# Kernel optimization log

Measured on AMD Instinct MI355X. Metric: run time of the kernel, lower is better.

## Reference

```python
import jax, jax.numpy as jnp
import numpy as np

N = 100000      # nodes
E = 3200000     # edges (avg degree 32)
IN = 256        # in_channels
HID = 32        # hidden (hard-coded in module)
OUT = 40        # out_channels / classes
BN_EPS = 1e-5


def gcn_conv(x, W, b, src, dst, n):
    # PyG GCNConv: h = x @ W; add self-loops; symmetric norm D^-1/2 A D^-1/2; aggregate; + bias
    h = x @ W                                   # [n, d_out]
    loop = jnp.arange(n)
    s = jnp.concatenate([src, loop])            # [E+n]
    d = jnp.concatenate([dst, loop])
    deg = jax.ops.segment_sum(jnp.ones_like(d, dtype=h.dtype), d, num_segments=n)
    dinv = jnp.where(deg > 0, jax.lax.rsqrt(deg), 0.0)
    norm = dinv[s] * dinv[d]                    # [E+n]
    msg = h[s] * norm[:, None]                  # gather + scale
    return jax.ops.segment_sum(msg, d, num_segments=n) + b


def setup_inputs() -> dict:
    key = jax.random.key(0)
    k = jax.random.split(key, 4)
    x = jax.random.normal(k[0], (N, IN), dtype=jnp.float32)
    edge_index = jax.random.randint(k[1], (2, E), 0, N, dtype=jnp.int64)
    W1 = jax.random.normal(k[2], (IN, HID), dtype=jnp.float32) / np.float32(np.sqrt(IN))
    b1 = jnp.zeros((HID,), jnp.float32)
    W2 = jax.random.normal(k[3], (HID, OUT), dtype=jnp.float32) / np.float32(np.sqrt(HID))
    b2 = jnp.zeros((OUT,), jnp.float32)
    return {"x": x, "edge_index": edge_index, "W1": W1, "b1": b1, "W2": W2, "b2": b2}


def reference(x, edge_index, W1, b1, W2, b2):
    src, dst = edge_index[0], edge_index[1]
    h = jax.nn.elu(gcn_conv(x, W1, b1, src, dst, N))
    # BatchNorm1d created fresh each forward: batch stats, gamma=1, beta=0 (biased var)
    mean = jnp.mean(h, axis=0)
    var = jnp.mean((h - mean) ** 2, axis=0)
    h = (h - mean) * jax.lax.rsqrt(var + BN_EPS)
    h = jax.nn.relu(h)
    # Dropout(p=0.2): identity in eval / deterministic reference
    out = gcn_conv(h, W2, b2, src, dst, N)
    return jax.nn.log_softmax(out, axis=-1)
```

## Files before the change

kernel.cpp:

```cpp
#include <hip/hip_runtime.h>
#include <math.h>

typedef unsigned int uint;
typedef unsigned short ushort;
typedef float v2f __attribute__((ext_vector_type(2)));

__device__ __forceinline__ v2f fp8lo_to_f32(uint u) {
    return __builtin_amdgcn_cvt_pk_f32_fp8((int)u, false);
}
__device__ __forceinline__ ushort f32x2_to_fp8(float a, float b) {
    return (ushort)(__builtin_amdgcn_cvt_pk_fp8_f32(a, b, 0, false) & 0xffff);
}

#define NBU 49
#define CELL 9216
#define BUCK_CAP (8 * CELL)

__global__ __launch_bounds__(256) void k_bin(
    const int* __restrict__ src, const int* __restrict__ dst,
    int* __restrict__ cur, uint* __restrict__ ebuf, int E) {
    __shared__ int hist[NBU], base_[NBU], off[NBU];
    int tid = threadIdx.x;
    if (tid < NBU) { hist[tid] = 0; off[tid] = 0; }
    __syncthreads();
    int e0 = blockIdx.x * 4096 + tid;
    int s_[16], d_[16];
#pragma unroll
    for (int j = 0; j < 16; ++j) {
        int e = e0 + j * 256;
        if (e < E) {
            s_[j] = src[e]; d_[j] = dst[e];
            atomicAdd(&hist[d_[j] >> 11], 1);
        } else d_[j] = -1;
    }
    __syncthreads();
    int seg = blockIdx.x & 7;
    if (tid < NBU && hist[tid])
        base_[tid] = atomicAdd(&cur[tid * 8 + seg], hist[tid]);
    __syncthreads();
#pragma unroll
    for (int j = 0; j < 16; ++j) {
        if (d_[j] >= 0) {
            int b = d_[j] >> 11;
            int p = base_[b] + atomicAdd(&off[b], 1);
            if (p < CELL)
                ebuf[(size_t)(b * 8 + seg) * CELL + p] =
                    ((uint)(d_[j] & 2047) << 17) | (uint)s_[j];
        }
    }
}

__global__ __launch_bounds__(1024) void k_sort(
    const int* __restrict__ cur, const uint* __restrict__ ebuf,
    uint* __restrict__ csr, int* __restrict__ rowstart, int* __restrict__ deg,
    float* __restrict__ dinv, int n) {
    __shared__ int cnt[2048];
    __shared__ int part[1024];
    int tid = threadIdx.x, b = blockIdx.x;
    cnt[2 * tid] = 0; cnt[2 * tid + 1] = 0;
    __syncthreads();
    int lens[8];
    for (int s = 0; s < 8; ++s) {
        int len = cur[b * 8 + s]; if (len > CELL) len = CELL; lens[s] = len;
        const uint* ep = ebuf + (size_t)(b * 8 + s) * CELL;
        for (int i = tid; i < len; i += 1024)
            atomicAdd(&cnt[ep[i] >> 17], 1);
    }
    __syncthreads();
    int c0 = cnt[2 * tid], c1 = cnt[2 * tid + 1];
    part[tid] = c0 + c1;
    __syncthreads();
    for (int o = 1; o < 1024; o <<= 1) {
        int v = (tid >= o) ? part[tid - o] : 0;
        __syncthreads();
        part[tid] += v;
        __syncthreads();
    }
    int excl = (tid == 0) ? 0 : part[tid - 1];
    int bucketBase = b * BUCK_CAP;
    int node0 = b * 2048 + 2 * tid;
    if (node0 < n) {
        rowstart[node0] = bucketBase + excl;
        deg[node0] = c0;
        dinv[node0] = rsqrtf((float)c0 + 1.0f);
    }
    if (node0 + 1 < n) {
        rowstart[node0 + 1] = bucketBase + excl + c0;
        deg[node0 + 1] = c1;
        dinv[node0 + 1] = rsqrtf((float)c1 + 1.0f);
    }
    __syncthreads();
    cnt[2 * tid] = excl;
    cnt[2 * tid + 1] = excl + c0;
    __syncthreads();
    for (int s = 0; s < 8; ++s) {
        const uint* ep = ebuf + (size_t)(b * 8 + s) * CELL;
        int len = lens[s];
        for (int i = tid; i < len; i += 1024) {
            uint v = ep[i];
            int p = atomicAdd(&cnt[v >> 17], 1);
            csr[bucketBase + p] = v & 0x1FFFFu;
        }
    }
}


__global__ __launch_bounds__(256) void k_gemm1(
    const float* __restrict__ x, const float* __restrict__ W,
    const float* __restrict__ dinv, ushort* __restrict__ h8, int n) {
    __shared__ float part[4 * 32 * 64];
    int lane = threadIdx.x & 63;
    int wv = __builtin_amdgcn_readfirstlane(threadIdx.x >> 6);
    int node0 = blockIdx.x * 64;
    int node = node0 + lane;
    int koff = wv * 64;

    float acc[32];
#pragma unroll
    for (int c = 0; c < 32; ++c) acc[c] = 0.f;
    if (node < n) {
        const float4* xr = (const float4*)(x + (size_t)node * 256 + koff);
#pragma unroll 4
        for (int j4 = 0; j4 < 16; ++j4) {
            float4 xv = xr[j4];
            const float* w0 = W + (koff + j4 * 4) * 32;
#pragma unroll
            for (int c = 0; c < 32; ++c) acc[c] += xv.x * w0[c];
#pragma unroll
            for (int c = 0; c < 32; ++c) acc[c] += xv.y * w0[32 + c];
#pragma unroll
            for (int c = 0; c < 32; ++c) acc[c] += xv.z * w0[64 + c];
#pragma unroll
            for (int c = 0; c < 32; ++c) acc[c] += xv.w * w0[96 + c];
        }
    }
    float* pw = part + wv * 2048 + lane;
#pragma unroll
    for (int c = 0; c < 32; ++c) pw[c * 64] = acc[c];
    __syncthreads();

    int rn = threadIdx.x >> 2;
    int cq = threadIdx.x & 3;
    int dnode = node0 + rn;
    if (dnode < n) {
        float di = dinv[dnode];
        ushort us[4];
#pragma unroll
        for (int half = 0; half < 4; ++half) {
            float v0 = 0.f, v1 = 0.f;
#pragma unroll
            for (int w = 0; w < 4; ++w) {
                v0 += part[w * 2048 + (cq * 8 + half * 2 + 0) * 64 + rn];
                v1 += part[w * 2048 + (cq * 8 + half * 2 + 1) * 64 + rn];
            }
            us[half] = f32x2_to_fp8(v0 * di, v1 * di);
        }
        uint2 p;
        p.x = (uint)us[0] | ((uint)us[1] << 16);
        p.y = (uint)us[2] | ((uint)us[3] << 16);
        *(uint2*)(h8 + (size_t)dnode * 16 + cq * 4) = p;
    }
}

__global__ __launch_bounds__(256) void k_agg1(
    const ushort* __restrict__ hs, const int* __restrict__ deg,
    const int* __restrict__ rowstart, const uint* __restrict__ csr,
    const float* __restrict__ dinv, const float* __restrict__ b1,
    ushort* __restrict__ y, float4* __restrict__ partials, int nChunks) {
    int g = threadIdx.x >> 4;
    int l = threadIdx.x & 15;
    float bx = b1[2*l], by = b1[2*l+1];
    float se = 0.f, so = 0.f, qe = 0.f, qo = 0.f;
    for (int chunk = blockIdx.x; chunk < nChunks; chunk += gridDim.x) {
        int d = chunk * 16 + g;
        v2f sv = fp8lo_to_f32(hs[(size_t)d * 16 + l]);
        float ax = sv.x, ay = sv.y;
        float cx = 0.f, cy = 0.f;
        const uint* row = csr + rowstart[d];
        int end = deg[d];
        int k = 0;
        for (; k + 4 <= end; k += 4) {
            uint s0 = row[k], s1 = row[k+1], s2 = row[k+2], s3 = row[k+3];
            v2f v0 = fp8lo_to_f32(hs[(size_t)s0 * 16 + l]);
            v2f v1 = fp8lo_to_f32(hs[(size_t)s1 * 16 + l]);
            v2f v2 = fp8lo_to_f32(hs[(size_t)s2 * 16 + l]);
            v2f v3 = fp8lo_to_f32(hs[(size_t)s3 * 16 + l]);
            ax += v0.x; ay += v0.y;
            cx += v1.x; cy += v1.y;
            ax += v2.x; ay += v2.y;
            cx += v3.x; cy += v3.y;
        }
        for (; k < end; ++k) {
            v2f v0 = fp8lo_to_f32(hs[(size_t)row[k] * 16 + l]);
            ax += v0.x; ay += v0.y;
        }
        float di = dinv[d];
        float v0 = di * (ax + cx) + bx;
        float v1 = di * (ay + cy) + by;
        v0 = v0 > 0.f ? v0 : expm1f(v0);
        v1 = v1 > 0.f ? v1 : expm1f(v1);
        y[(size_t)d * 16 + l] = f32x2_to_fp8(v0, v1);
        se += v0; so += v1; qe += v0*v0; qo += v1*v1;
    }
    __shared__ float4 red[256];
    red[threadIdx.x] = make_float4(se, so, qe, qo);
    __syncthreads();
    if (threadIdx.x < 16) {
        float4 a = make_float4(0.f, 0.f, 0.f, 0.f);
#pragma unroll
        for (int gg = 0; gg < 16; ++gg) {
            float4 t = red[gg * 16 + threadIdx.x];
            a.x += t.x; a.y += t.y; a.z += t.z; a.w += t.w;
        }
        partials[(size_t)blockIdx.x * 16 + threadIdx.x] = a;
    }
}

__global__ void k_red(const float4* __restrict__ partials,
                      float* __restrict__ stats, int nblk) {
    __shared__ float4 red[256];
    int t = threadIdx.x;
    float4 a = make_float4(0.f, 0.f, 0.f, 0.f);
    for (int i = t >> 4; i < nblk; i += 16) {
        float4 p = partials[(size_t)i * 16 + (t & 15)];
        a.x += p.x; a.y += p.y; a.z += p.z; a.w += p.w;
    }
    red[t] = a;
    __syncthreads();
    if (t < 16) {
        float4 s = make_float4(0.f, 0.f, 0.f, 0.f);
#pragma unroll
        for (int k = 0; k < 16; ++k) {
            float4 p = red[k * 16 + t];
            s.x += p.x; s.y += p.y; s.z += p.z; s.w += p.w;
        }
        stats[2*t] = s.x; stats[2*t+1] = s.y;
        stats[32+2*t] = s.z; stats[33+2*t] = s.w;
    }
}

__global__ void k_bn2(const ushort* __restrict__ y, const float* __restrict__ stats,
                      const float* __restrict__ dinv, ushort* __restrict__ h2s, int n) {
    int t = blockIdx.x * blockDim.x + threadIdx.x;
    if (t >= n * 16) return;
    int i = t >> 4, c2 = (t & 15) * 2;
    float invn = 1.0f / (float)n;
    float m0 = stats[c2] * invn,    m1 = stats[c2+1] * invn;
    float v0 = stats[32+c2] * invn - m0*m0;
    float v1 = stats[33+c2] * invn - m1*m1;
    float s0 = rsqrtf(v0 + 1e-5f), s1 = rsqrtf(v1 + 1e-5f);
    float di = dinv[i];
    v2f u = fp8lo_to_f32(y[t]);
    float a = (u.x - m0) * s0; a = a > 0.f ? a : 0.f; a *= di;
    float b = (u.y - m1) * s1; b = b > 0.f ? b : 0.f; b *= di;
    h2s[t] = f32x2_to_fp8(a, b);
}

__global__ __launch_bounds__(256) void k_agg2(
    const ushort* __restrict__ h2s, const int* __restrict__ deg,
    const int* __restrict__ rowstart, const uint* __restrict__ csr,
    const float* __restrict__ dinv, const float* __restrict__ W2,
    const float* __restrict__ b2, float* __restrict__ out, int n) {
    __shared__ float w2s[1280];
    __shared__ float b2s[40];
    __shared__ float tb[16][32];
    __shared__ float ob[16][40];
    for (int t = threadIdx.x; t < 1280; t += 256) w2s[t] = W2[t];
    if (threadIdx.x < 40) b2s[threadIdx.x] = b2[threadIdx.x];
    int g = threadIdx.x >> 4, l = threadIdx.x & 15;
    int d = blockIdx.x * 16 + g;
    v2f sv = fp8lo_to_f32(h2s[(size_t)d * 16 + l]);
    float ax = sv.x, ay = sv.y;
    float cx = 0.f, cy = 0.f;
    const uint* row = csr + rowstart[d];
    int end = deg[d];
    int k = 0;
    for (; k + 4 <= end; k += 4) {
        uint s0 = row[k], s1 = row[k+1], s2 = row[k+2], s3 = row[k+3];
        v2f v0 = fp8lo_to_f32(h2s[(size_t)s0 * 16 + l]);
        v2f v1 = fp8lo_to_f32(h2s[(size_t)s1 * 16 + l]);
        v2f v2 = fp8lo_to_f32(h2s[(size_t)s2 * 16 + l]);
        v2f v3 = fp8lo_to_f32(h2s[(size_t)s3 * 16 + l]);
        ax += v0.x; ay += v0.y;
        cx += v1.x; cy += v1.y;
        ax += v2.x; ay += v2.y;
        cx += v3.x; cy += v3.y;
    }
    for (; k < end; ++k) {
        v2f v0 = fp8lo_to_f32(h2s[(size_t)row[k] * 16 + l]);
        ax += v0.x; ay += v0.y;
    }
    float di = dinv[d];
    tb[g][2*l]   = di * (ax + cx);
    tb[g][2*l+1] = di * (ay + cy);
    __syncthreads();
    float o0 = b2s[l], o1 = b2s[l+16], o2 = (l < 8) ? b2s[l+32] : -1e30f;
#pragma unroll
    for (int c = 0; c < 32; ++c) {
        float tc = tb[g][c];
        o0 += tc * w2s[c*40 + l];
        o1 += tc * w2s[c*40 + l + 16];
        if (l < 8) o2 += tc * w2s[c*40 + l + 32];
    }
    ob[g][l] = o0; ob[g][l+16] = o1; if (l < 8) ob[g][l+32] = o2;
    __syncthreads();
    float mx = -1e30f;
#pragma unroll
    for (int j = 0; j < 40; ++j) mx = fmaxf(mx, ob[g][j]);
    float s = 0.f;
#pragma unroll
    for (int j = 0; j < 40; ++j) s += __expf(ob[g][j] - mx);
    float lse = mx + __logf(s);
    float* r = out + (size_t)d * 40;
    r[l] = o0 - lse; r[l+16] = o1 - lse; if (l < 8) r[l+32] = o2 - lse;
}


extern "C" void kernel_launch(void* const* d_in, const int* in_sizes, int n_in,
                              void* d_out, int out_size, void* d_ws, size_t ws_size,
                              hipStream_t stream) {
    const float* x  = (const float*)d_in[0];
    const int*   ei = (const int*)d_in[1];
    const float* W1 = (const float*)d_in[2];
    const float* b1 = (const float*)d_in[3];
    const float* W2 = (const float*)d_in[4];
    const float* b2 = (const float*)d_in[5];

    int n = in_sizes[0] / 256;
    int E = in_sizes[1] / 2;
    const int* src = ei;
    const int* dst = ei + E;

    char*   base    = (char*)d_ws;
    ushort* hs8     = (ushort*)base;
    ushort* y       = (ushort*)(base + (size_t)n * 32);
    ushort* h2s     = (ushort*)(base + (size_t)n * 64);
    float*  dinv    = (float*) (base + (size_t)n * 96);
    int*    deg     = (int*)   (base + (size_t)n * 100);
    int*    rowstart= (int*)   (base + (size_t)n * 104);
    float*  stats   = (float*) (base + (size_t)n * 108);
    int*    cur     = (int*)   (base + (size_t)n * 108 + 256);
    float4* partials= (float4*)(base + (size_t)n * 108 + 2304);
    uint*   ebuf    = (uint*)  (base + (size_t)n * 108 + 2304 + 524288);
    size_t  ebufB   = (size_t)NBU * 8 * CELL * 4;
    uint*   csr     = (uint*)  ((char*)ebuf + ebufB);
    float*  out     = (float*)d_out;

    const int B = 256;
    int nChunks = n / 16;
    const int AGG1_GRID = 2048;

    hipMemsetAsync(cur, 0, NBU * 8 * sizeof(int), stream);

    k_bin <<<(E + 4095) / 4096, B, 0, stream>>>(src, dst, cur, ebuf, E);
    k_sort<<<NBU, 1024, 0, stream>>>(cur, ebuf, csr, rowstart, deg, dinv, n);

    k_gemm1<<<(n + 63) / 64, B, 0, stream>>>(x, W1, dinv, hs8, n);
    k_agg1 <<<AGG1_GRID, B, 0, stream>>>(hs8, deg, rowstart, csr, dinv, b1, y,
                                         partials, nChunks);
    k_red  <<<1, 256, 0, stream>>>(partials, stats, AGG1_GRID);

    k_bn2<<<(n * 16 + B - 1) / B, B, 0, stream>>>(y, stats, dinv, h2s, n);

    k_agg2<<<nChunks, B, 0, stream>>>(h2s, deg, rowstart, csr, dinv, W2, b2, out, n);
}
```

Measured before the change: 442.9 us.

## Gather 8 fp8 channels per lane in aggregation, 4 lanes per node

Both aggregation kernels now assign 4 lanes per destination node, each loading a uint2 (8 fp8 channels) per neighbor instead of 16 lanes loading 2 channels each. The goal is fewer memory instructions and more nodes in flight per wave for the random gathers. The layer-1 BN statistics reduction is reworked with wave shuffles and a 1024-thread final reduction, and the grid becomes one block per 64 nodes. In layer 2 the output GEMM and log-softmax use per-lane 10-wide register tiles with shuffle-based max and sum. In exchange each lane holds more registers and the softmax relies on cross-lane shuffles.

```diff
diff --git a/kernel.cpp b/kernel.cpp
--- a/kernel.cpp
+++ b/kernel.cpp
@@ -8,9 +8,20 @@
 __device__ __forceinline__ v2f fp8lo_to_f32(uint u) {
     return __builtin_amdgcn_cvt_pk_f32_fp8((int)u, false);
 }
+__device__ __forceinline__ v2f fp8hi_to_f32(uint u) {
+    return __builtin_amdgcn_cvt_pk_f32_fp8((int)u, true);
+}
 __device__ __forceinline__ ushort f32x2_to_fp8(float a, float b) {
     return (ushort)(__builtin_amdgcn_cvt_pk_fp8_f32(a, b, 0, false) & 0xffff);
 }
+
+#define UNPACK8(r, f)                                                  \
+    {                                                                  \
+        v2f p0_ = fp8lo_to_f32((r).x), p1_ = fp8hi_to_f32((r).x);      \
+        v2f p2_ = fp8lo_to_f32((r).y), p3_ = fp8hi_to_f32((r).y);      \
+        f[0] += p0_.x; f[1] += p0_.y; f[2] += p1_.x; f[3] += p1_.y;    \
+        f[4] += p2_.x; f[5] += p2_.y; f[6] += p3_.x; f[7] += p3_.y;    \
+    }
 
 #define NBU 49
 #define CELL 9216
@@ -166,76 +177,97 @@
     const ushort* __restrict__ hs, const int* __restrict__ deg,
     const int* __restrict__ rowstart, const uint* __restrict__ csr,
     const float* __restrict__ dinv, const float* __restrict__ b1,
-    ushort* __restrict__ y, float4* __restrict__ partials, int nChunks) {
-    int g = threadIdx.x >> 4;
-    int l = threadIdx.x & 15;
-    float bx = b1[2*l], by = b1[2*l+1];
-    float se = 0.f, so = 0.f, qe = 0.f, qo = 0.f;
-    for (int chunk = blockIdx.x; chunk < nChunks; chunk += gridDim.x) {
-        int d = chunk * 16 + g;
-        v2f sv = fp8lo_to_f32(hs[(size_t)d * 16 + l]);
-        float ax = sv.x, ay = sv.y;
-        float cx = 0.f, cy = 0.f;
+    ushort* __restrict__ y, float* __restrict__ partials, int n) {
+    int tid = threadIdx.x;
+    int l4 = tid & 3;
+    int g  = tid >> 2;
+    int d  = blockIdx.x * 64 + g;
+    float sa[8], qa[8];
+#pragma unroll
+    for (int j = 0; j < 8; ++j) { sa[j] = 0.f; qa[j] = 0.f; }
+    if (d < n) {
+        float a[8], c[8];
+#pragma unroll
+        for (int j = 0; j < 8; ++j) { a[j] = 0.f; c[j] = 0.f; }
+        uint2 sr = *((const uint2*)(hs + (size_t)d * 16) + l4);
+        UNPACK8(sr, a);
         const uint* row = csr + rowstart[d];
         int end = deg[d];
         int k = 0;
         for (; k + 4 <= end; k += 4) {
             uint s0 = row[k], s1 = row[k+1], s2 = row[k+2], s3 = row[k+3];
-            v2f v0 = fp8lo_to_f32(hs[(size_t)s0 * 16 + l]);
-            v2f v1 = fp8lo_to_f32(hs[(size_t)s1 * 16 + l]);
-            v2f v2 = fp8lo_to_f32(hs[(size_t)s2 * 16 + l]);
-            v2f v3 = fp8lo_to_f32(hs[(size_t)s3 * 16 + l]);
-            ax += v0.x; ay += v0.y;
-            cx += v1.x; cy += v1.y;
-            ax += v2.x; ay += v2.y;
-            cx += v3.x; cy += v3.y;
+            uint2 r0 = *((const uint2*)(hs + (size_t)s0 * 16) + l4);
+            uint2 r1 = *((const uint2*)(hs + (size_t)s1 * 16) + l4);
+            uint2 r2 = *((const uint2*)(hs + (size_t)s2 * 16) + l4);
+            uint2 r3 = *((const uint2*)(hs + (size_t)s3 * 16) + l4);
+            UNPACK8(r0, a); UNPACK8(r1, c);
+            UNPACK8(r2, a); UNPACK8(r3, c);
         }
         for (; k < end; ++k) {
-            v2f v0 = fp8lo_to_f32(hs[(size_t)row[k] * 16 + l]);
-            ax += v0.x; ay += v0.y;
+            uint2 r = *((const uint2*)(hs + (size_t)row[k] * 16) + l4);
+            UNPACK8(r, a);
         }
         float di = dinv[d];
-        float v0 = di * (ax + cx) + bx;
-        float v1 = di * (ay + cy) + by;
-        v0 = v0 > 0.f ? v0 : expm1f(v0);
-        v1 = v1 > 0.f ? v1 : expm1f(v1);
-        y[(size_t)d * 16 + l] = f32x2_to_fp8(v0, v1);
-        se += v0; so += v1; qe += v0*v0; qo += v1*v1;
-    }
-    __shared__ float4 red[256];
-    red[threadIdx.x] = make_float4(se, so, qe, qo);
-    __syncthreads();
-    if (threadIdx.x < 16) {
-        float4 a = make_float4(0.f, 0.f, 0.f, 0.f);
-#pragma unroll
-        for (int gg = 0; gg < 16; ++gg) {
-            float4 t = red[gg * 16 + threadIdx.x];
-            a.x += t.x; a.y += t.y; a.z += t.z; a.w += t.w;
-        }
-        partials[(size_t)blockIdx.x * 16 + threadIdx.x] = a;
-    }
-}
-
-__global__ void k_red(const float4* __restrict__ partials,
-                      float* __restrict__ stats, int nblk) {
-    __shared__ float4 red[256];
+        float4 bA = *(const float4*)(b1 + l4 * 8);
+        float4 bB = *(const float4*)(b1 + l4 * 8 + 4);
+        float bv[8] = {bA.x, bA.y, bA.z, bA.w, bB.x, bB.y, bB.z, bB.w};
+        float vv[8];
+#pragma unroll
+        for (int j = 0; j < 8; ++j) {
+            float v = di * (a[j] + c[j]) + bv[j];
+            v = v > 0.f ? v : expm1f(v);
+            vv[j] = v; sa[j] = v; qa[j] = v * v;
+        }
+        ushort u0 = f32x2_to_fp8(vv[0], vv[1]);
+        ushort u1 = f32x2_to_fp8(vv[2], vv[3]);
+        ushort u2 = f32x2_to_fp8(vv[4], vv[5]);
+        ushort u3 = f32x2_to_fp8(vv[6], vv[7]);
+        uint2 pw;
+        pw.x = (uint)u0 | ((uint)u1 << 16);
+        pw.y = (uint)u2 | ((uint)u3 << 16);
+        *((uint2*)(y + (size_t)d * 16) + l4) = pw;
+    }
+#pragma unroll
+    for (int m = 4; m <= 32; m <<= 1) {
+#pragma unroll
+        for (int j = 0; j < 8; ++j) {
+            sa[j] += __shfl_xor(sa[j], m, 64);
+            qa[j] += __shfl_xor(qa[j], m, 64);
+        }
+    }
+    __shared__ float wred[4][4][16];
+    int lane = tid & 63, wv = tid >> 6;
+    if (lane < 4) {
+#pragma unroll
+        for (int j = 0; j < 8; ++j) {
+            wred[wv][lane][j]     = sa[j];
+            wred[wv][lane][8 + j] = qa[j];
+        }
+    }
+    __syncthreads();
+    if (tid < 64) {
+        int l4g = tid >> 4, slot = tid & 15;
+        partials[(size_t)blockIdx.x * 64 + tid] =
+            wred[0][l4g][slot] + wred[1][l4g][slot] +
+            wred[2][l4g][slot] + wred[3][l4g][slot];
+    }
+}
+
+__global__ __launch_bounds__(1024) void k_red(
+    const float* __restrict__ partials, float* __restrict__ stats, int nblk) {
+    __shared__ float red[1024];
     int t = threadIdx.x;
-    float4 a = make_float4(0.f, 0.f, 0.f, 0.f);
-    for (int i = t >> 4; i < nblk; i += 16) {
-        float4 p = partials[(size_t)i * 16 + (t & 15)];
-        a.x += p.x; a.y += p.y; a.z += p.z; a.w += p.w;
-    }
+    int j = t & 63, w = t >> 6;
+    float a = 0.f;
+    for (int i = w; i < nblk; i += 16) a += partials[(size_t)i * 64 + j];
     red[t] = a;
     __syncthreads();
-    if (t < 16) {
-        float4 s = make_float4(0.f, 0.f, 0.f, 0.f);
-#pragma unroll
-        for (int k = 0; k < 16; ++k) {
-            float4 p = red[k * 16 + t];
-            s.x += p.x; s.y += p.y; s.z += p.z; s.w += p.w;
-        }
-        stats[2*t] = s.x; stats[2*t+1] = s.y;
-        stats[32+2*t] = s.z; stats[33+2*t] = s.w;
+    if (t < 64) {
+        float v = 0.f;
+#pragma unroll
+        for (int kk = 0; kk < 16; ++kk) v += red[kk * 64 + t];
+        int l4g = t >> 4, slot = t & 15, c = l4g * 8 + (slot & 7);
+        stats[(slot < 8) ? c : (32 + c)] = v;
     }
 }
 
@@ -263,56 +295,70 @@
     const float* __restrict__ b2, float* __restrict__ out, int n) {
     __shared__ float w2s[1280];
     __shared__ float b2s[40];
-    __shared__ float tb[16][32];
-    __shared__ float ob[16][40];
-    for (int t = threadIdx.x; t < 1280; t += 256) w2s[t] = W2[t];
-    if (threadIdx.x < 40) b2s[threadIdx.x] = b2[threadIdx.x];
-    int g = threadIdx.x >> 4, l = threadIdx.x & 15;
-    int d = blockIdx.x * 16 + g;
-    v2f sv = fp8lo_to_f32(h2s[(size_t)d * 16 + l]);
-    float ax = sv.x, ay = sv.y;
-    float cx = 0.f, cy = 0.f;
-    const uint* row = csr + rowstart[d];
-    int end = deg[d];
-    int k = 0;
-    for (; k + 4 <= end; k += 4) {
-        uint s0 = row[k], s1 = row[k+1], s2 = row[k+2], s3 = row[k+3];
-        v2f v0 = fp8lo_to_f32(h2s[(size_t)s0 * 16 + l]);
-        v2f v1 = fp8lo_to_f32(h2s[(size_t)s1 * 16 + l]);
-        v2f v2 = fp8lo_to_f32(h2s[(size_t)s2 * 16 + l]);
-        v2f v3 = fp8lo_to_f32(h2s[(size_t)s3 * 16 + l]);
-        ax += v0.x; ay += v0.y;
-        cx += v1.x; cy += v1.y;
-        ax += v2.x; ay += v2.y;
-        cx += v3.x; cy += v3.y;
-    }
-    for (; k < end; ++k) {
-        v2f v0 = fp8lo_to_f32(h2s[(size_t)row[k] * 16 + l]);
-        ax += v0.x; ay += v0.y;
-    }
-    float di = dinv[d];
-    tb[g][2*l]   = di * (ax + cx);
-    tb[g][2*l+1] = di * (ay + cy);
-    __syncthreads();
-    float o0 = b2s[l], o1 = b2s[l+16], o2 = (l < 8) ? b2s[l+32] : -1e30f;
-#pragma unroll
-    for (int c = 0; c < 32; ++c) {
-        float tc = tb[g][c];
-        o0 += tc * w2s[c*40 + l];
-        o1 += tc * w2s[c*40 + l + 16];
-        if (l < 8) o2 += tc * w2s[c*40 + l + 32];
-    }
-    ob[g][l] = o0; ob[g][l+16] = o1; if (l < 8) ob[g][l+32] = o2;
-    __syncthreads();
-    float mx = -1e30f;
-#pragma unroll
-    for (int j = 0; j < 40; ++j) mx = fmaxf(mx, ob[g][j]);
+    __shared__ float tb[64][33];
+    int tid = threadIdx.x;
+    for (int t = tid; t < 1280; t += 256) w2s[t] = W2[t];
+    if (tid < 40) b2s[tid] = b2[tid];
+    int l4 = tid & 3, g = tid >> 2;
+    int d = blockIdx.x * 64 + g;
+    if (d < n) {
+        float a[8], c[8];
+#pragma unroll
+        for (int j = 0; j < 8; ++j) { a[j] = 0.f; c[j] = 0.f; }
+        uint2 sr = *((const uint2*)(h2s + (size_t)d * 16) + l4);
+        UNPACK8(sr, a);
+        const uint* row = csr + rowstart[d];
+        int end = deg[d];
+        int k = 0;
+        for (; k + 4 <= end; k += 4) {
+            uint s0 = row[k], s1 = row[k+1], s2 = row[k+2], s3 = row[k+3];
+            uint2 r0 = *((const uint2*)(h2s + (size_t)s0 * 16) + l4);
+            uint2 r1 = *((const uint2*)(h2s + (size_t)s1 * 16) + l4);
+            uint2 r2 = *((const uint2*)(h2s + (size_t)s2 * 16) + l4);
+            uint2 r3 = *((const uint2*)(h2s + (size_t)s3 * 16) + l4);
+            UNPACK8(r0, a); UNPACK8(r1, c);
+            UNPACK8(r2, a); UNPACK8(r3, c);
+        }
+        for (; k < end; ++k) {
+            uint2 r = *((const uint2*)(h2s + (size_t)row[k] * 16) + l4);
+            UNPACK8(r, a);
+        }
+        float di = dinv[d];
+#pragma unroll
+        for (int j = 0; j < 8; ++j) tb[g][l4 * 8 + j] = di * (a[j] + c[j]);
+    }
+    __syncthreads();
+    float o[10];
+    const float* bp = b2s + l4 * 10;
+#pragma unroll
+    for (int m = 0; m < 10; ++m) o[m] = bp[m];
+#pragma unroll
+    for (int cc = 0; cc < 32; ++cc) {
+        float tc = tb[g][cc];
+        const float* wr = w2s + cc * 40 + l4 * 10;
+#pragma unroll
+        for (int m = 0; m < 10; ++m) o[m] += tc * wr[m];
+    }
+    float mx = o[0];
+#pragma unroll
+    for (int m = 1; m < 10; ++m) mx = fmaxf(mx, o[m]);
+    mx = fmaxf(mx, __shfl_xor(mx, 1, 64));
+    mx = fmaxf(mx, __shfl_xor(mx, 2, 64));
     float s = 0.f;
 #pragma unroll
-    for (int j = 0; j < 40; ++j) s += __expf(ob[g][j] - mx);
+    for (int m = 0; m < 10; ++m) s += __expf(o[m] - mx);
+    s += __shfl_xor(s, 1, 64);
+    s += __shfl_xor(s, 2, 64);
     float lse = mx + __logf(s);
-    float* r = out + (size_t)d * 40;
-    r[l] = o0 - lse; r[l+16] = o1 - lse; if (l < 8) r[l+32] = o2 - lse;
+    if (d < n) {
+        float* r = out + (size_t)d * 40 + l4 * 10;
+#pragma unroll
+        for (int m = 0; m < 10; m += 2) {
+            float2 wv;
+            wv.x = o[m] - lse; wv.y = o[m+1] - lse;
+            *(float2*)(r + m) = wv;
+        }
+    }
 }
 
 
@@ -340,15 +386,14 @@
     int*    rowstart= (int*)   (base + (size_t)n * 104);
     float*  stats   = (float*) (base + (size_t)n * 108);
     int*    cur     = (int*)   (base + (size_t)n * 108 + 256);
-    float4* partials= (float4*)(base + (size_t)n * 108 + 2304);
+    float*  partials= (float*) (base + (size_t)n * 108 + 2304);
     uint*   ebuf    = (uint*)  (base + (size_t)n * 108 + 2304 + 524288);
     size_t  ebufB   = (size_t)NBU * 8 * CELL * 4;
     uint*   csr     = (uint*)  ((char*)ebuf + ebufB);
     float*  out     = (float*)d_out;
 
     const int B = 256;
-    int nChunks = n / 16;
-    const int AGG1_GRID = 2048;
+    int nb64 = (n + 63) / 64;
 
     hipMemsetAsync(cur, 0, NBU * 8 * sizeof(int), stream);
 
@@ -356,11 +401,11 @@
     k_sort<<<NBU, 1024, 0, stream>>>(cur, ebuf, csr, rowstart, deg, dinv, n);
 
     k_gemm1<<<(n + 63) / 64, B, 0, stream>>>(x, W1, dinv, hs8, n);
-    k_agg1 <<<AGG1_GRID, B, 0, stream>>>(hs8, deg, rowstart, csr, dinv, b1, y,
-                                         partials, nChunks);
-    k_red  <<<1, 256, 0, stream>>>(partials, stats, AGG1_GRID);
+    k_agg1 <<<nb64, B, 0, stream>>>(hs8, deg, rowstart, csr, dinv, b1, y,
+                                    partials, n);
+    k_red  <<<1, 1024, 0, stream>>>(partials, stats, nb64);
 
     k_bn2<<<(n * 16 + B - 1) / B, B, 0, stream>>>(y, stats, dinv, h2s, n);
 
-    k_agg2<<<nChunks, B, 0, stream>>>(h2s, deg, rowstart, csr, dinv, W2, b2, out, n);
-}
+    k_agg2<<<nb64, B, 0, stream>>>(h2s, deg, rowstart, csr, dinv, W2, b2, out, n);
+}
```

New measurement: 407.3 us. 8.0% less time.
